# Kernel tuning notes

Hardware: AMD Instinct MI355X
Metric: run time of the kernel (lower is better)

Reference implementation:

```python
import jax, jax.numpy as jnp
import numpy as np
from jax.scipy.fft import dct as jdct, idct as jidct

B, C, L = 512, 64, 512
KEEP_L, KEEP_C = 256, 32          # int(L*0.5), int(C*0.5)
KEEP_L2, KEEP_C2 = 128, 16        # int(KEEP_L*0.5), int(KEEP_C*0.5)


def dct2(x2d):
    # scipy: dct(dct(x, axis=0, norm='ortho'), axis=1, norm='ortho') on (B*C, L)
    return jdct(jdct(x2d, norm='ortho', axis=0), norm='ortho', axis=1)


def idct2(x2d):
    # scipy: idct(idct(X, axis=1, norm='ortho'), axis=0, norm='ortho')
    return jidct(jidct(x2d, norm='ortho', axis=1), norm='ortho', axis=0)


def setup_inputs() -> dict:
    key = jax.random.key(0)
    ks = jax.random.split(key, 7)
    x = jax.random.normal(ks[0], (B, C, L), dtype=jnp.float32)
    W1 = jax.random.normal(ks[1], (L, L), dtype=jnp.float32) / np.sqrt(L)
    b1 = jax.random.normal(ks[2], (L,), dtype=jnp.float32) * 0.01
    W2 = jax.random.normal(ks[3], (KEEP_L, KEEP_L), dtype=jnp.float32) / np.sqrt(KEEP_L)
    b2 = jax.random.normal(ks[4], (KEEP_L,), dtype=jnp.float32) * 0.01
    W3 = jax.random.normal(ks[5], (KEEP_L2, KEEP_L2), dtype=jnp.float32) / np.sqrt(KEEP_L2)
    b3 = jax.random.normal(ks[6], (KEEP_L2,), dtype=jnp.float32) * 0.01
    return {"x": x, "W1": W1, "b1": b1, "W2": W2, "b2": b2, "W3": W3, "b3": b3}


def reference(x, W1, b1, W2, b2, W3, b3):
    Bx, Cx, Lx = x.shape
    # 2D DCT over the flattened (B*C, L) view
    T = dct2(x.reshape(-1, Lx)).reshape(Bx, Cx, Lx)

    # branch 1: Linear over full L
    y1 = T @ W1.T + b1

    # branch 2: Linear over truncated coeffs, zero-pad back to (B, C, L)
    t1 = T[:, :KEEP_C, :KEEP_L]
    y2 = jnp.pad(t1 @ W2.T + b2, ((0, 0), (0, Cx - KEEP_C), (0, Lx - KEEP_L)))

    # branch 3: further truncation
    t2 = T[:, :KEEP_C2, :KEEP_L2]
    y3 = jnp.pad(t2 @ W3.T + b3, ((0, 0), (0, Cx - KEEP_C2), (0, Lx - KEEP_L2)))

    out = jnp.concatenate(
        [idct2(y.reshape(-1, Lx)).reshape(Bx, Cx, Lx) for y in (y1, y2, y3)],
        axis=-1,
    )  # (B, C, 3L)
    return out
```

## Files before the change

### kernel.cpp

```cpp
#include <hip/hip_runtime.h>
#include <cstddef>


#define PI_D 3.14159265358979323846

typedef _Float16 h8 __attribute__((ext_vector_type(8)));
typedef _Float16 h4 __attribute__((ext_vector_type(4)));
typedef float f4 __attribute__((ext_vector_type(4)));

#define MFMA16(a, b, c) __builtin_amdgcn_mfma_f32_16x16x32_f16(a, b, c, 0, 0, 0)

__global__ __launch_bounds__(256) void megafill_k(
    float* __restrict__ F, _Float16* __restrict__ Cmh, _Float16* __restrict__ Smnh,
    _Float16* __restrict__ CmTh, _Float16* __restrict__ SmTh,
    float* __restrict__ v1, float* __restrict__ w2, float* __restrict__ w3,
    const float* __restrict__ b1, const float* __restrict__ b2,
    const float* __restrict__ b3, float* __restrict__ c1, float* __restrict__ c2,
    float* __restrict__ c3) {
  const int blk = blockIdx.x;
  const int tid = threadIdx.x;
  if (blk < 1024) {
    int idx = blk * 256 + tid;
    int k = idx >> 9, m = idx & 511;
    int a = (k * (2 * m + 1)) & 2047;
    float ang = (float)(a * (PI_D / 1024.0));
    float s = (k == 0) ? 0.04419417382415922f : 0.0625f;
    F[idx] = s * cosf(ang);
  } else if (blk < 2048) {
    int idx = (blk - 1024) * 256 + tid;
    int t = idx >> 9, v = idx & 511;
    int a = (t * (2 * v + 1)) & 2047;
    float ang = (float)(a * (PI_D / 1024.0));
    float c = cosf(ang), s = sinf(ang);
    Cmh[idx] = (_Float16)c;
    Smnh[idx] = (_Float16)(-s);
    CmTh[v * 512 + t] = (_Float16)c;
    SmTh[v * 512 + t] = (_Float16)s;
  } else if (blk < 2176) {
    int n = (blk - 2048) * 256 + tid;
    const double s1 = 0.005524271728019903;
    const double s2 = 0.0078125;
    double th = (2 * n + 1) * (PI_D / 65536.0);
    double c = cos(th), s = sin(th);
    double Dr = 1.0 - c, Di = -s;
    double dd = Dr * Dr + Di * Di;
    double Nr = 1.0, Ni = (n & 1) ? 1.0 : -1.0;
    double vre = (Nr * Dr + Ni * Di) / dd;
    v1[n] = (float)(s2 * vre + (s1 - s2));
    int m64 = (2 * n + 1) & 2047;
    double a64 = m64 * (PI_D / 1024.0);
    double D64r = 1.0 - cos(a64), D64i = -sin(a64);
    double d64 = D64r * D64r + D64i * D64i;
    double Gr = (Nr * D64r + Ni * D64i) / d64;
    double Gi = (Ni * D64r - Nr * D64i) / d64;
    int m32 = (2 * n + 1) & 4095;
    double a32 = m32 * (PI_D / 2048.0);
    double S32nr = 1.0 - cos(a32), S32ni = -sin(a32);
    double S32r = (S32nr * Dr + S32ni * Di) / dd;
    double S32i = (S32ni * Dr - S32nr * Di) / dd;
    w2[n] = (float)(s2 * (S32r * Gr - S32i * Gi) + (s1 - s2));
    int m16 = (2 * n + 1) & 8191;
    double a16 = m16 * (PI_D / 4096.0);
    double S16nr = 1.0 - cos(a16), S16ni = -sin(a16);
    double S16r = (S16nr * Dr + S16ni * Di) / dd;
    double S16i = (S16ni * Dr - S16nr * Di) / dd;
    w3[n] = (float)(s2 * (S16r * Gr - S16i * Gi) + (s1 - s2));
  } else {
    int gid = (blk - 2176) * 4 + (tid >> 6);
    int lane = tid & 63;
    int branch = gid >> 9;
    int l = gid & 511;
    int K = 512 >> branch;
    const float* b = (branch == 0) ? b1 : (branch == 1) ? b2 : b3;
    float acc = 0.f;
    for (int m = lane; m < K; m += 64) {
      int a = (m * (2 * l + 1)) & 2047;
      float s = (m == 0) ? 0.04419417382415922f : 0.0625f;
      acc += s * cosf((float)(a * (PI_D / 1024.0))) * b[m];
    }
#pragma unroll
    for (int o = 32; o > 0; o >>= 1) acc += __shfl_down(acc, o, 64);
    if (lane == 0) {
      float* c = (branch == 0) ? c1 : (branch == 1) ? c2 : c3;
      c[l] = acc;
    }
  }
}

__global__ void conv_xh_k(const float* __restrict__ X, _Float16* __restrict__ Xh) {
  int i = blockIdx.x * 256 + threadIdx.x;
  float4 v = ((const float4*)X)[i];
  h4 o;
  o[0] = (_Float16)v.x; o[1] = (_Float16)v.y; o[2] = (_Float16)v.z; o[3] = (_Float16)v.w;
  ((h4*)Xh)[i] = o;
}

__device__ void sgemm_dev(_Float16* As, _Float16* Bs, int bx, int by,
                          const float* __restrict__ A, int lda, int transA,
                          const float* __restrict__ B, int ldb,
                          float* __restrict__ Cf, _Float16* __restrict__ C16,
                          int K, float scale) {
  const int tid = threadIdx.x;
  const int lane = tid & 63;
  const int wm = (tid >> 6) & 1, wn = tid >> 7;
  const int m0 = by * 128, n0 = bx * 128;
  const int fm = lane & 15, fko = (lane >> 4) * 8;
  f4 acc[4][4] = {};
  for (int k0 = 0; k0 < K; k0 += 32) {
    if (transA) {
#pragma unroll
      for (int i = 0; i < 4; i++) {
        int idx4 = tid + i * 256;
        int kk = idx4 & 31, mc = (idx4 >> 5) * 4;
        float4 v = *(const float4*)&A[(size_t)(k0 + kk) * lda + m0 + mc];
        As[(mc + 0) * 40 + kk] = (_Float16)v.x;
        As[(mc + 1) * 40 + kk] = (_Float16)v.y;
        As[(mc + 2) * 40 + kk] = (_Float16)v.z;
        As[(mc + 3) * 40 + kk] = (_Float16)v.w;
      }
    } else {
#pragma unroll
      for (int i = 0; i < 4; i++) {
        int idx4 = tid + i * 256;
        int mm = idx4 >> 3, kc = (idx4 & 7) * 4;
        float4 v = *(const float4*)&A[(size_t)(m0 + mm) * lda + k0 + kc];
        h4 o;
        o[0] = (_Float16)v.x; o[1] = (_Float16)v.y; o[2] = (_Float16)v.z; o[3] = (_Float16)v.w;
        *(h4*)&As[mm * 40 + kc] = o;
      }
    }
#pragma unroll
    for (int i = 0; i < 4; i++) {
      int idx4 = tid + i * 256;
      int kk = idx4 & 31, nc = (idx4 >> 5) * 4;
      float4 v = *(const float4*)&B[(size_t)(k0 + kk) * ldb + n0 + nc];
      Bs[(nc + 0) * 40 + kk] = (_Float16)v.x;
      Bs[(nc + 1) * 40 + kk] = (_Float16)v.y;
      Bs[(nc + 2) * 40 + kk] = (_Float16)v.z;
      Bs[(nc + 3) * 40 + kk] = (_Float16)v.w;
    }
    __syncthreads();
    h8 af[4], bf[4];
#pragma unroll
    for (int i = 0; i < 4; i++) af[i] = *(const h8*)&As[(wm * 64 + i * 16 + fm) * 40 + fko];
#pragma unroll
    for (int j = 0; j < 4; j++) bf[j] = *(const h8*)&Bs[(wn * 64 + j * 16 + fm) * 40 + fko];
#pragma unroll
    for (int i = 0; i < 4; i++)
#pragma unroll
      for (int j = 0; j < 4; j++) acc[i][j] = MFMA16(af[i], bf[j], acc[i][j]);
    __syncthreads();
  }
  const int er = (lane >> 4) * 4, ec = lane & 15;
#pragma unroll
  for (int i = 0; i < 4; i++) {
    int gr0 = m0 + wm * 64 + i * 16 + er;
#pragma unroll
    for (int j = 0; j < 4; j++) {
      int gc = n0 + wn * 64 + j * 16 + ec;
#pragma unroll
      for (int r = 0; r < 4; r++) {
        size_t off = (size_t)(gr0 + r) * 512 + gc;
        if (C16) C16[off] = (_Float16)(acc[i][j][r] * scale);
        else Cf[off] = acc[i][j][r];
      }
    }
  }
}

__global__ __launch_bounds__(256) void sgemm_stage1_k(
    const float* __restrict__ W1, const float* __restrict__ W2,
    const float* __restrict__ W3, const float* __restrict__ F,
    float* __restrict__ Pst, float* __restrict__ Q2, float* __restrict__ Q3) {
  __shared__ _Float16 As[128 * 40];
  __shared__ _Float16 Bs[128 * 40];
  int id = blockIdx.x;
  if (id < 16) {
    sgemm_dev(As, Bs, id & 3, id >> 2, W1, 512, 1, F, 512, Pst, nullptr, 512, 1.f);
  } else if (id < 24) {
    int j = id - 16;
    sgemm_dev(As, Bs, j & 3, j >> 2, W2, 256, 0, F, 512, Q2, nullptr, 256, 1.f);
  } else {
    int j = id - 24;
    sgemm_dev(As, Bs, j & 3, j >> 2, W3, 128, 0, F, 512, Q3, nullptr, 128, 1.f);
  }
}

__global__ __launch_bounds__(256) void sgemm_stage2_k(
    const float* __restrict__ F, const float* __restrict__ Pst,
    const float* __restrict__ Q2, const float* __restrict__ Q3,
    _Float16* __restrict__ M1T, _Float16* __restrict__ M2T,
    _Float16* __restrict__ M3T) {
  __shared__ _Float16 As[128 * 40];
  __shared__ _Float16 Bs[128 * 40];
  int id = blockIdx.x;
  if (id < 16) {
    sgemm_dev(As, Bs, id & 3, id >> 2, Pst, 512, 1, F, 512, nullptr, M1T, 512, 1.f);
  } else if (id < 32) {
    int j = id - 16;
    sgemm_dev(As, Bs, j & 3, j >> 2, F, 512, 1, Q2, 512, nullptr, M2T, 256, 0.0078125f);
  } else {
    int j = id - 32;
    sgemm_dev(As, Bs, j & 3, j >> 2, F, 512, 1, Q3, 512, nullptr, M3T, 128, 0.0078125f);
  }
}

__global__ __launch_bounds__(256) void transpose2_h_k(
    const _Float16* __restrict__ in0, _Float16* __restrict__ out0, int C0,
    const _Float16* __restrict__ in1, _Float16* __restrict__ out1, int C1,
    int xsplit, int R) {
  __shared__ _Float16 t[64][66];
  const _Float16* in;
  _Float16* out;
  int C, bx;
  if ((int)blockIdx.x < xsplit) { in = in0; out = out0; C = C0; bx = blockIdx.x; }
  else { in = in1; out = out1; C = C1; bx = blockIdx.x - xsplit; }
  int tid = threadIdx.x;
  int bxo = bx * 64;
  int by = blockIdx.y * 64;
  int cx = (tid & 15) * 4;
  int ry = tid >> 4;
#pragma unroll
  for (int p = 0; p < 4; p++) {
    int r = ry + p * 16;
    h4 v = *(const h4*)&in[(size_t)(by + r) * C + bxo + cx];
    t[r][cx + 0] = v[0]; t[r][cx + 1] = v[1]; t[r][cx + 2] = v[2]; t[r][cx + 3] = v[3];
  }
  __syncthreads();
#pragma unroll
  for (int p = 0; p < 4; p++) {
    int r2 = ry + p * 16;
    h4 v;
    v[0] = t[cx + 0][r2]; v[1] = t[cx + 1][r2]; v[2] = t[cx + 2][r2]; v[3] = t[cx + 3][r2];
    *(h4*)&out[(size_t)(bxo + r2) * R + by + cx] = v;
  }
}

__device__ __forceinline__ void async16(const _Float16* g, _Float16* l) {
  __builtin_amdgcn_global_load_lds((const __attribute__((address_space(1))) void*)g,
                                   (__attribute__((address_space(3))) void*)l, 16, 0, 0);
}

template <int MODE>
__device__ void gemm_dev(_Float16* As, _Float16* Bs, int bx, int by,
                         const _Float16* __restrict__ A1, const _Float16* __restrict__ A2,
                         const _Float16* __restrict__ B1, const _Float16* __restrict__ B2,
                         void* __restrict__ C1, void* __restrict__ C2, int ldc, int coff,
                         const float* __restrict__ u, const float* __restrict__ wvec,
                         int sb, int tb) {
  constexpr bool DA = (MODE == 1 || MODE == 2);
  constexpr bool DB = (MODE == 1);
  const int tid = threadIdx.x;
  const int lane = tid & 63;
  const int wm = (tid >> 6) & 1, wn = tid >> 7;
  const int m0 = by * 128, n0 = bx * 128;
  const int srow = tid >> 2, scol = (tid & 3) * 8;
  const int mask = (1 << sb) - 1;
  f4 acc[4][4] = {};
  f4 acc2[4][4] = {};
  const int fm = lane & 15, fko = (lane >> 4) * 8;
  for (int k0 = 0; k0 < 512; k0 += 32) {
#pragma unroll
    for (int i = 0; i < 2; i++) {
      int r = m0 + i * 64 + srow;
      int pr = ((r >> sb) << tb) | (r & mask);
      async16(A1 + (size_t)pr * 512 + k0 + scol, &As[i * 2048 + tid * 8]);
      if constexpr (DA)
        async16(A2 + (size_t)pr * 512 + k0 + scol, &As[4096 + i * 2048 + tid * 8]);
      int rb = n0 + i * 64 + srow;
      async16(B1 + (size_t)rb * 512 + k0 + scol, &Bs[i * 2048 + tid * 8]);
      if constexpr (DB)
        async16(B2 + (size_t)rb * 512 + k0 + scol, &Bs[4096 + i * 2048 + tid * 8]);
    }
    __syncthreads();
    h8 af[4], bf[4], af2[4], bf2[4];
#pragma unroll
    for (int i = 0; i < 4; i++) {
      int ro = (wm * 64 + i * 16 + fm) * 32 + fko;
      af[i] = *(const h8*)&As[ro];
      if constexpr (DA) af2[i] = *(const h8*)&As[4096 + ro];
    }
#pragma unroll
    for (int j = 0; j < 4; j++) {
      int co = (wn * 64 + j * 16 + fm) * 32 + fko;
      bf[j] = *(const h8*)&Bs[co];
      if constexpr (DB) bf2[j] = *(const h8*)&Bs[4096 + co];
    }
#pragma unroll
    for (int i = 0; i < 4; i++)
#pragma unroll
      for (int j = 0; j < 4; j++) {
        acc[i][j] = MFMA16(af[i], bf[j], acc[i][j]);
        if constexpr (MODE == 1) acc[i][j] = MFMA16(af2[i], bf2[j], acc[i][j]);
        if constexpr (MODE == 2) acc2[i][j] = MFMA16(af2[i], bf[j], acc2[i][j]);
      }
    __syncthreads();
  }
  const int er = (lane >> 4) * 4, ec = lane & 15;
#pragma unroll
  for (int i = 0; i < 4; i++) {
    int gr0 = m0 + wm * 64 + i * 16 + er;
#pragma unroll
    for (int j = 0; j < 4; j++) {
      int gc = n0 + wn * 64 + j * 16 + ec;
#pragma unroll
      for (int r = 0; r < 4; r++) {
        size_t off = (size_t)(gr0 + r) * ldc + coff + gc;
        if constexpr (MODE == 3) {
          ((float*)C1)[off] = acc[i][j][r] + u[gr0 + r] * wvec[gc];
        } else if constexpr (MODE == 2) {
          ((_Float16*)C1)[off] = (_Float16)acc[i][j][r];
          ((_Float16*)C2)[off] = (_Float16)acc2[i][j][r];
        } else if constexpr (MODE == 1) {
          float v = acc[i][j][r];
          if ((gr0 + r) == 0 && gc < 512) v *= 0.5f;
          ((_Float16*)C1)[off] = (_Float16)v;
        } else {
          ((_Float16*)C1)[off] = (_Float16)acc[i][j][r];
        }
      }
    }
  }
}

template <int MODE>
__global__ __launch_bounds__(256) void mfma_gemm_k(
    const _Float16* __restrict__ A1, const _Float16* __restrict__ A2,
    const _Float16* __restrict__ B1, const _Float16* __restrict__ B2,
    void* __restrict__ C1, void* __restrict__ C2, int ldc, int coff,
    const float* __restrict__ u, const float* __restrict__ wvec, int sb, int tb) {
  __shared__ __align__(16) _Float16 As[((MODE == 1 || MODE == 2) ? 2 : 1) * 4096];
  __shared__ __align__(16) _Float16 Bs[(MODE == 1 ? 2 : 1) * 4096];
  gemm_dev<MODE>(As, Bs, blockIdx.x, blockIdx.y, A1, A2, B1, B2, C1, C2, ldc, coff,
                 u, wvec, sb, tb);
}

__global__ __launch_bounds__(256) void gemm0_pair_k(
    const _Float16* __restrict__ Zh, const _Float16* __restrict__ M2T,
    const _Float16* __restrict__ M3T, _Float16* __restrict__ Y2,
    _Float16* __restrict__ Y3) {
  __shared__ __align__(16) _Float16 As[4096];
  __shared__ __align__(16) _Float16 Bs[4096];
  if ((int)blockIdx.y < 128)
    gemm_dev<0>(As, Bs, blockIdx.x, blockIdx.y, Zh, nullptr, M2T, nullptr, Y2, nullptr,
                512, 0, nullptr, nullptr, 30, 30);
  else
    gemm_dev<0>(As, Bs, blockIdx.x, blockIdx.y - 128, Zh, nullptr, M3T, nullptr, Y3,
                nullptr, 512, 0, nullptr, nullptr, 4, 5);
}

__global__ __launch_bounds__(256) void gemm2_pair_k(
    const _Float16* __restrict__ CmTh, const _Float16* __restrict__ SmTh,
    const _Float16* __restrict__ Y2T, const _Float16* __restrict__ Y3T,
    _Float16* __restrict__ Pc2, _Float16* __restrict__ Ps2,
    _Float16* __restrict__ Pc3, _Float16* __restrict__ Ps3) {
  __shared__ __align__(16) _Float16 As[2 * 4096];
  __shared__ __align__(16) _Float16 Bs[4096];
  if ((int)blockIdx.x < 128)
    gemm_dev<2>(As, Bs, blockIdx.x, blockIdx.y, CmTh, SmTh, Y2T, nullptr, Pc2, Ps2,
                16384, 0, nullptr, nullptr, 30, 30);
  else
    gemm_dev<2>(As, Bs, blockIdx.x - 128, blockIdx.y, CmTh, SmTh, Y3T, nullptr, Pc3,
                Ps3, 8192, 0, nullptr, nullptr, 30, 30);
}

__global__ __launch_bounds__(256) void modmfma_k(
    const _Float16* __restrict__ Xh, _Float16* __restrict__ zc,
    _Float16* __restrict__ zs) {
  __shared__ _Float16 Bs[256 * 72];
  __shared__ _Float16 Ac[32 * 72];
  __shared__ _Float16 As[32 * 72];
  const int tid = threadIdx.x;
  const int lane = tid & 63;
  const int wid = tid >> 6;
  const int vp = blockIdx.y;
  const int l0 = blockIdx.x * 256;
  const float sc = 0.0078125f;
  {
    int r = lane;
    int u = r & 31;
    int n = (r < 32) ? ((u << 10) + vp) : ((u << 10) + 1023 - vp);
    const _Float16* src = Xh + (size_t)n * 512 + l0 + wid * 64;
#pragma unroll
    for (int i = 0; i < 8; i++) {
      h8 v = *(const h8*)(src + i * 8);
      int lb = wid * 64 + i * 8;
#pragma unroll
      for (int e = 0; e < 8; e++) Bs[(lb + e) * 72 + r] = v[e];
    }
  }
  for (int idx = tid; idx < 2048; idx += 256) {
    int kk = idx & 63, j = idx >> 6;
    int u = kk & 31;
    int n = (kk < 32) ? ((u << 10) + vp) : ((u << 10) + 1023 - vp);
    int a = (j * (2 * n + 1)) & 131071;
    float sv, cv;
    __sincosf((float)(a * (PI_D / 65536.0)), &sv, &cv);
    Ac[j * 72 + kk] = (_Float16)(cv * sc);
    As[j * 72 + kk] = (_Float16)(((kk < 32) ? sv : -sv) * sc);
  }
  __syncthreads();
  const int fm = lane & 15, fko = (lane >> 4) * 8;
  f4 accc[2][4] = {};
  f4 accs[2][4] = {};
#pragma unroll
  for (int ks = 0; ks < 2; ks++) {
    int ko = ks * 32 + fko;
    h8 afc[2], afs[2], bf[4];
#pragma unroll
    for (int i = 0; i < 2; i++) {
      afc[i] = *(const h8*)&Ac[(i * 16 + fm) * 72 + ko];
      afs[i] = *(const h8*)&As[(i * 16 + fm) * 72 + ko];
    }
#pragma unroll
    for (int j = 0; j < 4; j++)
      bf[j] = *(const h8*)&Bs[(wid * 64 + j * 16 + fm) * 72 + ko];
#pragma unroll
    for (int i = 0; i < 2; i++)
#pragma unroll
      for (int j = 0; j < 4; j++) {
        accc[i][j] = MFMA16(afc[i], bf[j], accc[i][j]);
        accs[i][j] = MFMA16(afs[i], bf[j], accs[i][j]);
      }
  }
  const int er = (lane >> 4) * 4, ec = lane & 15;
#pragma unroll
  for (int i = 0; i < 2; i++)
#pragma unroll
    for (int j = 0; j < 4; j++)
#pragma unroll
      for (int r = 0; r < 4; r++) {
        int row = i * 16 + er + r;
        int col = l0 + wid * 64 + j * 16 + ec;
        size_t off = (size_t)vp * 16384 + row * 512 + col;
        zc[off] = (_Float16)accc[i][j][r];
        zs[off] = (_Float16)accs[i][j][r];
      }
}

template <int JC>
__device__ void demod_dev(char* smemraw, const _Float16* __restrict__ Pc,
                          const _Float16* __restrict__ Ps,
                          const float* __restrict__ wv, const float* __restrict__ cw,
                          float* __restrict__ out, int coff) {
  constexpr int K2 = 2 * JC;
  constexpr int ST = K2 + 8;
  _Float16* Bs = (_Float16*)smemraw;
  _Float16* At = (_Float16*)(smemraw + (size_t)256 * ST * 2);
  const int tid = threadIdx.x;
  const int lane = tid & 63;
  const int wid = tid >> 6;
  const int vp = blockIdx.y;
  const int l0 = blockIdx.x * 256;
  {
    constexpr int CPL = 64 / K2;
    int r = lane & (K2 - 1);
    int chunk = wid * CPL + (CPL == 1 ? 0 : (lane >> 5));
    int lb = chunk * K2;
    const _Float16* src = (r < JC ? Pc + (size_t)vp * (JC * 512) + r * 512
                                  : Ps + (size_t)vp * (JC * 512) + (r - JC) * 512) +
                          l0 + lb;
#pragma unroll
    for (int i = 0; i < K2 / 8; i++) {
      h8 v = *(const h8*)(src + i * 8);
#pragma unroll
      for (int e = 0; e < 8; e++) Bs[(lb + i * 8 + e) * ST + r] = v[e];
    }
  }
  for (int idx = tid; idx < 64 * K2; idx += 256) {
    int kk = idx & (K2 - 1), m = idx / K2;
    int ab = m >> 5, u = m & 31;
    int n = ab ? ((u << 10) + 1023 - vp) : ((u << 10) + vp);
    int twon = 2 * n + 1;
    float val;
    if (kk < JC) {
      int a = (kk * twon) & 131071;
      val = cosf((float)(a * (PI_D / 65536.0)));
    } else {
      int a = ((kk - JC) * twon) & 131071;
      float sv = sinf((float)(a * (PI_D / 65536.0)));
      val = ab ? sv : -sv;
    }
    At[m * ST + kk] = (_Float16)val;
  }
  __syncthreads();
  const int fm = lane & 15, fko = (lane >> 4) * 8;
  f4 acc[4][4] = {};
#pragma unroll
  for (int ks = 0; ks < K2 / 32; ks++) {
    int ko = ks * 32 + fko;
    h8 af[4], bf[4];
#pragma unroll
    for (int i = 0; i < 4; i++) af[i] = *(const h8*)&At[(i * 16 + fm) * ST + ko];
#pragma unroll
    for (int j = 0; j < 4; j++) bf[j] = *(const h8*)&Bs[(wid * 64 + j * 16 + fm) * ST + ko];
#pragma unroll
    for (int i = 0; i < 4; i++)
#pragma unroll
      for (int j = 0; j < 4; j++) acc[i][j] = MFMA16(af[i], bf[j], acc[i][j]);
  }
  const int er = (lane >> 4) * 4, ec = lane & 15;
#pragma unroll
  for (int i = 0; i < 4; i++)
#pragma unroll
    for (int j = 0; j < 4; j++) {
      int col = l0 + wid * 64 + j * 16 + ec;
      float cl = cw[col];
#pragma unroll
      for (int r = 0; r < 4; r++) {
        int m = i * 16 + er + r;
        int ab = m >> 5, u = m & 31;
        int n = ab ? ((u << 10) + 1023 - vp) : ((u << 10) + vp);
        out[(size_t)n * 1536 + coff + col] = acc[i][j][r] + wv[n] * cl;
      }
    }
}

__global__ __launch_bounds__(256) void demod_pair_k(
    const _Float16* __restrict__ Pc2, const _Float16* __restrict__ Ps2,
    const float* __restrict__ w2v, const float* __restrict__ c2,
    const _Float16* __restrict__ Pc3, const _Float16* __restrict__ Ps3,
    const float* __restrict__ w3v, const float* __restrict__ c3,
    float* __restrict__ out) {
  __shared__ __align__(16) char smem[256 * 72 * 2 + 64 * 72 * 2];
  if (blockIdx.z == 0)
    demod_dev<32>(smem, Pc2, Ps2, w2v, c2, out, 512);
  else
    demod_dev<16>(smem, Pc3, Ps3, w3v, c3, out, 1024);
}

extern "C" void kernel_launch(void* const* d_in, const int* in_sizes, int n_in,
                              void* d_out, int out_size, void* d_ws, size_t ws_size,
                              hipStream_t stream) {
  const float* X  = (const float*)d_in[0];
  const float* W1 = (const float*)d_in[1];
  const float* b1 = (const float*)d_in[2];
  const float* W2 = (const float*)d_in[3];
  const float* b2 = (const float*)d_in[4];
  const float* W3 = (const float*)d_in[5];
  const float* b3 = (const float*)d_in[6];
  float* out = (float*)d_out;
  char* w = (char*)d_ws;
  const size_t MB = 1024 * 1024;

  float* F    = (float*)(w);
  float* v1   = (float*)(w + 9 * MB);
  float* w2v  = (float*)(w + 9 * MB + 131072);
  float* w3v  = (float*)(w + 9 * MB + 262144);
  float* c1   = (float*)(w + 9 * MB + 393216);
  float* c2   = (float*)(w + 9 * MB + 395264);
  float* c3   = (float*)(w + 9 * MB + 397312);
  float* Pst  = (float*)(w + 10 * MB);
  _Float16* CmTh = (_Float16*)(w + 11 * MB);
  _Float16* SmTh = (_Float16*)(w + 11 * MB + 524288);
  _Float16* Cmh  = (_Float16*)(w + 12 * MB);
  _Float16* Smnh = (_Float16*)(w + 12 * MB + 524288);
  _Float16* M1T  = (_Float16*)(w + 13 * MB);
  _Float16* M2T  = (_Float16*)(w + 13 * MB + 524288);
  _Float16* M3T  = (_Float16*)(w + 14 * MB);
  float* Q2      = (float*)(w + 14 * MB + 524288);
  float* Q3      = (float*)(w + 15 * MB);
  _Float16* Xh   = (_Float16*)(w + 16 * MB);
  _Float16* zc   = (_Float16*)(w + 48 * MB);
  _Float16* zs   = (_Float16*)(w + 64 * MB);
  _Float16* Pc2h = (_Float16*)(w + 48 * MB);
  _Float16* Ps2h = (_Float16*)(w + 64 * MB);
  _Float16* Pc3h = (_Float16*)(w + 104 * MB);
  _Float16* Ps3h = (_Float16*)(w + 112 * MB);
  _Float16* zcT  = (_Float16*)(w + 80 * MB);
  _Float16* zsT  = (_Float16*)(w + 96 * MB);
  _Float16* Y2T  = (_Float16*)(w + 80 * MB);
  _Float16* Y3T  = (_Float16*)(w + 96 * MB);
  _Float16* Zh   = (_Float16*)(w + 112 * MB);
  _Float16* Y2   = (_Float16*)(w + 128 * MB);
  _Float16* Y3   = (_Float16*)(w + 144 * MB);

  megafill_k<<<2560, 256, 0, stream>>>(F, Cmh, Smnh, CmTh, SmTh, v1, w2v, w3v,
                                       b1, b2, b3, c1, c2, c3);
  sgemm_stage1_k<<<28, 256, 0, stream>>>(W1, W2, W3, F, Pst, Q2, Q3);
  sgemm_stage2_k<<<48, 256, 0, stream>>>(F, Pst, Q2, Q3, M1T, M2T, M3T);
  conv_xh_k<<<16384, 256, 0, stream>>>(X, Xh);
  modmfma_k<<<dim3(2, 512), 256, 0, stream>>>(Xh, zc, zs);
  transpose2_h_k<<<dim3(512, 8), 256, 0, stream>>>(zc, zcT, 16384, zs, zsT, 16384,
                                                   256, 512);
  mfma_gemm_k<1><<<dim3(128, 4), 256, 0, stream>>>(Cmh, Smnh, zcT, zsT, Zh, nullptr,
                                                   16384, 0, nullptr, nullptr, 30, 30);
  gemm0_pair_k<<<dim3(4, 192), 256, 0, stream>>>(Zh, M2T, M3T, Y2, Y3);
  transpose2_h_k<<<dim3(384, 8), 256, 0, stream>>>(Y2, Y2T, 16384, Y3, Y3T, 8192,
                                                   256, 512);
  gemm2_pair_k<<<dim3(192, 4), 256, 0, stream>>>(CmTh, SmTh, Y2T, Y3T, Pc2h, Ps2h,
                                                 Pc3h, Ps3h);
  demod_pair_k<<<dim3(2, 512, 2), 256, 0, stream>>>(Pc2h, Ps2h, w2v, c2, Pc3h, Ps3h,
                                                    w3v, c3, out);
  mfma_gemm_k<3><<<dim3(4, 256), 256, 0, stream>>>(Xh, nullptr, M1T, nullptr, out,
                                                   nullptr, 1536, 0, v1, c1, 30, 30);
}
```

Before: 588.5 us.

## Fuse setup kernels, drop transposes via k-major B loads, merge final GEMM

The DCT matrix F is now computed on the fly inside the small setup GEMMs instead of being materialized. The fill and stage-1 GEMMs are merged into one launch, and the X conversion and stage-2 GEMMs into another. The two transpose kernels are removed: the MFMA GEMMs read k-major B directly, scattering it into a swizzled LDS layout to avoid bank conflicts. The branch-1 output GEMM is folded into the trio GEMM launch. This cuts launch count and the transpose memory traffic, at the cost of scalar LDS scatter stores, recomputed cosines, and heavier tail blocks in the merged grids.

Measured after the change: 650.9 us. 10.6% more time.

```diff
diff --git a/kernel.cpp b/kernel.cpp
--- a/kernel.cpp
+++ b/kernel.cpp
@@ -10,24 +10,120 @@
 
 #define MFMA16(a, b, c) __builtin_amdgcn_mfma_f32_16x16x32_f16(a, b, c, 0, 0, 0)
 
-__global__ __launch_bounds__(256) void megafill_k(
-    float* __restrict__ F, _Float16* __restrict__ Cmh, _Float16* __restrict__ Smnh,
+__device__ __forceinline__ float Fval(int k, int m) {
+  int a = (k * (2 * m + 1)) & 2047;
+  float s = (k == 0) ? 0.04419417382415922f : 0.0625f;
+  return s * cosf((float)(a * (PI_D / 1024.0)));
+}
+
+__device__ void sgemm_dev(_Float16* As, _Float16* Bs, int bx, int by,
+                          const float* __restrict__ A, int lda, int amode,
+                          const float* __restrict__ B, int ldb, int bmode,
+                          float* __restrict__ Cf, _Float16* __restrict__ C16,
+                          int K, float scale) {
+  const int tid = threadIdx.x;
+  const int lane = tid & 63;
+  const int wm = (tid >> 6) & 1, wn = tid >> 7;
+  const int m0 = by * 128, n0 = bx * 128;
+  const int fm = lane & 15, fko = (lane >> 4) * 8;
+  f4 acc[4][4] = {};
+  for (int k0 = 0; k0 < K; k0 += 32) {
+    if (amode == 1) {
+#pragma unroll
+      for (int i = 0; i < 4; i++) {
+        int idx4 = tid + i * 256;
+        int kk = idx4 & 31, mc = (idx4 >> 5) * 4;
+        float4 v = *(const float4*)&A[(size_t)(k0 + kk) * lda + m0 + mc];
+        As[(mc + 0) * 40 + kk] = (_Float16)v.x;
+        As[(mc + 1) * 40 + kk] = (_Float16)v.y;
+        As[(mc + 2) * 40 + kk] = (_Float16)v.z;
+        As[(mc + 3) * 40 + kk] = (_Float16)v.w;
+      }
+    } else if (amode == 0) {
+#pragma unroll
+      for (int i = 0; i < 4; i++) {
+        int idx4 = tid + i * 256;
+        int mm = idx4 >> 3, kc = (idx4 & 7) * 4;
+        float4 v = *(const float4*)&A[(size_t)(m0 + mm) * lda + k0 + kc];
+        h4 o;
+        o[0] = (_Float16)v.x; o[1] = (_Float16)v.y; o[2] = (_Float16)v.z; o[3] = (_Float16)v.w;
+        *(h4*)&As[mm * 40 + kc] = o;
+      }
+    } else {
+#pragma unroll
+      for (int i = 0; i < 4; i++) {
+        int idx4 = tid + i * 256;
+        int kk = idx4 & 31, mc = (idx4 >> 5) * 4;
+#pragma unroll
+        for (int e = 0; e < 4; e++)
+          As[(mc + e) * 40 + kk] = (_Float16)Fval(k0 + kk, m0 + mc + e);
+      }
+    }
+    if (bmode == 0) {
+#pragma unroll
+      for (int i = 0; i < 4; i++) {
+        int idx4 = tid + i * 256;
+        int kk = idx4 & 31, nc = (idx4 >> 5) * 4;
+        float4 v = *(const float4*)&B[(size_t)(k0 + kk) * ldb + n0 + nc];
+        Bs[(nc + 0) * 40 + kk] = (_Float16)v.x;
+        Bs[(nc + 1) * 40 + kk] = (_Float16)v.y;
+        Bs[(nc + 2) * 40 + kk] = (_Float16)v.z;
+        Bs[(nc + 3) * 40 + kk] = (_Float16)v.w;
+      }
+    } else {
+#pragma unroll
+      for (int i = 0; i < 4; i++) {
+        int idx4 = tid + i * 256;
+        int kk = idx4 & 31, nc = (idx4 >> 5) * 4;
+#pragma unroll
+        for (int e = 0; e < 4; e++)
+          Bs[(nc + e) * 40 + kk] = (_Float16)Fval(k0 + kk, n0 + nc + e);
+      }
+    }
+    __syncthreads();
+    h8 af[4], bf[4];
+#pragma unroll
+    for (int i = 0; i < 4; i++) af[i] = *(const h8*)&As[(wm * 64 + i * 16 + fm) * 40 + fko];
+#pragma unroll
+    for (int j = 0; j < 4; j++) bf[j] = *(const h8*)&Bs[(wn * 64 + j * 16 + fm) * 40 + fko];
+#pragma unroll
+    for (int i = 0; i < 4; i++)
+#pragma unroll
+      for (int j = 0; j < 4; j++) acc[i][j] = MFMA16(af[i], bf[j], acc[i][j]);
+    __syncthreads();
+  }
+  const int er = (lane >> 4) * 4, ec = lane & 15;
+#pragma unroll
+  for (int i = 0; i < 4; i++) {
+    int gr0 = m0 + wm * 64 + i * 16 + er;
+#pragma unroll
+    for (int j = 0; j < 4; j++) {
+      int gc = n0 + wn * 64 + j * 16 + ec;
+#pragma unroll
+      for (int r = 0; r < 4; r++) {
+        size_t off = (size_t)(gr0 + r) * 512 + gc;
+        if (C16) C16[off] = (_Float16)(acc[i][j][r] * scale);
+        else Cf[off] = acc[i][j][r];
+      }
+    }
+  }
+}
+
+__global__ __launch_bounds__(256) void mega1_k(
+    _Float16* __restrict__ Cmh, _Float16* __restrict__ Smnh,
     _Float16* __restrict__ CmTh, _Float16* __restrict__ SmTh,
     float* __restrict__ v1, float* __restrict__ w2, float* __restrict__ w3,
     const float* __restrict__ b1, const float* __restrict__ b2,
     const float* __restrict__ b3, float* __restrict__ c1, float* __restrict__ c2,
-    float* __restrict__ c3) {
+    float* __restrict__ c3, const float* __restrict__ W1,
+    const float* __restrict__ W2, const float* __restrict__ W3,
+    float* __restrict__ Pst, float* __restrict__ Q2, float* __restrict__ Q3) {
+  __shared__ _Float16 As[128 * 40];
+  __shared__ _Float16 Bs[128 * 40];
   const int blk = blockIdx.x;
   const int tid = threadIdx.x;
   if (blk < 1024) {
     int idx = blk * 256 + tid;
-    int k = idx >> 9, m = idx & 511;
-    int a = (k * (2 * m + 1)) & 2047;
-    float ang = (float)(a * (PI_D / 1024.0));
-    float s = (k == 0) ? 0.04419417382415922f : 0.0625f;
-    F[idx] = s * cosf(ang);
-  } else if (blk < 2048) {
-    int idx = (blk - 1024) * 256 + tid;
     int t = idx >> 9, v = idx & 511;
     int a = (t * (2 * v + 1)) & 2047;
     float ang = (float)(a * (PI_D / 1024.0));
@@ -36,8 +132,8 @@
     Smnh[idx] = (_Float16)(-s);
     CmTh[v * 512 + t] = (_Float16)c;
     SmTh[v * 512 + t] = (_Float16)s;
-  } else if (blk < 2176) {
-    int n = (blk - 2048) * 256 + tid;
+  } else if (blk < 1152) {
+    int n = (blk - 1024) * 256 + tid;
     const double s1 = 0.005524271728019903;
     const double s2 = 0.0078125;
     double th = (2 * n + 1) * (PI_D / 65536.0);
@@ -65,174 +161,60 @@
     double S16r = (S16nr * Dr + S16ni * Di) / dd;
     double S16i = (S16ni * Dr - S16nr * Di) / dd;
     w3[n] = (float)(s2 * (S16r * Gr - S16i * Gi) + (s1 - s2));
-  } else {
-    int gid = (blk - 2176) * 4 + (tid >> 6);
+  } else if (blk < 1536) {
+    int gid = (blk - 1152) * 4 + (tid >> 6);
     int lane = tid & 63;
     int branch = gid >> 9;
     int l = gid & 511;
     int K = 512 >> branch;
     const float* b = (branch == 0) ? b1 : (branch == 1) ? b2 : b3;
     float acc = 0.f;
-    for (int m = lane; m < K; m += 64) {
-      int a = (m * (2 * l + 1)) & 2047;
-      float s = (m == 0) ? 0.04419417382415922f : 0.0625f;
-      acc += s * cosf((float)(a * (PI_D / 1024.0))) * b[m];
-    }
+    for (int m = lane; m < K; m += 64) acc += Fval(m, l) * b[m];
 #pragma unroll
     for (int o = 32; o > 0; o >>= 1) acc += __shfl_down(acc, o, 64);
     if (lane == 0) {
       float* c = (branch == 0) ? c1 : (branch == 1) ? c2 : c3;
       c[l] = acc;
     }
-  }
-}
-
-__global__ void conv_xh_k(const float* __restrict__ X, _Float16* __restrict__ Xh) {
-  int i = blockIdx.x * 256 + threadIdx.x;
-  float4 v = ((const float4*)X)[i];
-  h4 o;
-  o[0] = (_Float16)v.x; o[1] = (_Float16)v.y; o[2] = (_Float16)v.z; o[3] = (_Float16)v.w;
-  ((h4*)Xh)[i] = o;
-}
-
-__device__ void sgemm_dev(_Float16* As, _Float16* Bs, int bx, int by,
-                          const float* __restrict__ A, int lda, int transA,
-                          const float* __restrict__ B, int ldb,
-                          float* __restrict__ Cf, _Float16* __restrict__ C16,
-                          int K, float scale) {
-  const int tid = threadIdx.x;
-  const int lane = tid & 63;
-  const int wm = (tid >> 6) & 1, wn = tid >> 7;
-  const int m0 = by * 128, n0 = bx * 128;
-  const int fm = lane & 15, fko = (lane >> 4) * 8;
-  f4 acc[4][4] = {};
-  for (int k0 = 0; k0 < K; k0 += 32) {
-    if (transA) {
-#pragma unroll
-      for (int i = 0; i < 4; i++) {
-        int idx4 = tid + i * 256;
-        int kk = idx4 & 31, mc = (idx4 >> 5) * 4;
-        float4 v = *(const float4*)&A[(size_t)(k0 + kk) * lda + m0 + mc];
-        As[(mc + 0) * 40 + kk] = (_Float16)v.x;
-        As[(mc + 1) * 40 + kk] = (_Float16)v.y;
-        As[(mc + 2) * 40 + kk] = (_Float16)v.z;
-        As[(mc + 3) * 40 + kk] = (_Float16)v.w;
-      }
+  } else {
+    int id = blk - 1536;
+    if (id < 16) {
+      sgemm_dev(As, Bs, id & 3, id >> 2, W1, 512, 1, nullptr, 0, 1, Pst, nullptr, 512, 1.f);
+    } else if (id < 24) {
+      int j = id - 16;
+      sgemm_dev(As, Bs, j & 3, j >> 2, W2, 256, 0, nullptr, 0, 1, Q2, nullptr, 256, 1.f);
     } else {
-#pragma unroll
-      for (int i = 0; i < 4; i++) {
-        int idx4 = tid + i * 256;
-        int mm = idx4 >> 3, kc = (idx4 & 7) * 4;
-        float4 v = *(const float4*)&A[(size_t)(m0 + mm) * lda + k0 + kc];
-        h4 o;
-        o[0] = (_Float16)v.x; o[1] = (_Float16)v.y; o[2] = (_Float16)v.z; o[3] = (_Float16)v.w;
-        *(h4*)&As[mm * 40 + kc] = o;
-      }
-    }
-#pragma unroll
-    for (int i = 0; i < 4; i++) {
-      int idx4 = tid + i * 256;
-      int kk = idx4 & 31, nc = (idx4 >> 5) * 4;
-      float4 v = *(const float4*)&B[(size_t)(k0 + kk) * ldb + n0 + nc];
-      Bs[(nc + 0) * 40 + kk] = (_Float16)v.x;
-      Bs[(nc + 1) * 40 + kk] = (_Float16)v.y;
-      Bs[(nc + 2) * 40 + kk] = (_Float16)v.z;
-      Bs[(nc + 3) * 40 + kk] = (_Float16)v.w;
-    }
-    __syncthreads();
-    h8 af[4], bf[4];
-#pragma unroll
-    for (int i = 0; i < 4; i++) af[i] = *(const h8*)&As[(wm * 64 + i * 16 + fm) * 40 + fko];
-#pragma unroll
-    for (int j = 0; j < 4; j++) bf[j] = *(const h8*)&Bs[(wn * 64 + j * 16 + fm) * 40 + fko];
-#pragma unroll
-    for (int i = 0; i < 4; i++)
-#pragma unroll
-      for (int j = 0; j < 4; j++) acc[i][j] = MFMA16(af[i], bf[j], acc[i][j]);
-    __syncthreads();
-  }
-  const int er = (lane >> 4) * 4, ec = lane & 15;
-#pragma unroll
-  for (int i = 0; i < 4; i++) {
-    int gr0 = m0 + wm * 64 + i * 16 + er;
-#pragma unroll
-    for (int j = 0; j < 4; j++) {
-      int gc = n0 + wn * 64 + j * 16 + ec;
-#pragma unroll
-      for (int r = 0; r < 4; r++) {
-        size_t off = (size_t)(gr0 + r) * 512 + gc;
-        if (C16) C16[off] = (_Float16)(acc[i][j][r] * scale);
-        else Cf[off] = acc[i][j][r];
-      }
-    }
-  }
-}
-
-__global__ __launch_bounds__(256) void sgemm_stage1_k(
-    const float* __restrict__ W1, const float* __restrict__ W2,
-    const float* __restrict__ W3, const float* __restrict__ F,
-    float* __restrict__ Pst, float* __restrict__ Q2, float* __restrict__ Q3) {
+      int j = id - 24;
+      sgemm_dev(As, Bs, j & 3, j >> 2, W3, 128, 0, nullptr, 0, 1, Q3, nullptr, 128, 1.f);
+    }
+  }
+}
+
+__global__ __launch_bounds__(256) void mega2_k(
+    const float* __restrict__ X, _Float16* __restrict__ Xh,
+    const float* __restrict__ Pst, const float* __restrict__ Q2,
+    const float* __restrict__ Q3, _Float16* __restrict__ M1T,
+    _Float16* __restrict__ M2T, _Float16* __restrict__ M3T) {
   __shared__ _Float16 As[128 * 40];
   __shared__ _Float16 Bs[128 * 40];
-  int id = blockIdx.x;
-  if (id < 16) {
-    sgemm_dev(As, Bs, id & 3, id >> 2, W1, 512, 1, F, 512, Pst, nullptr, 512, 1.f);
-  } else if (id < 24) {
-    int j = id - 16;
-    sgemm_dev(As, Bs, j & 3, j >> 2, W2, 256, 0, F, 512, Q2, nullptr, 256, 1.f);
+  const int blk = blockIdx.x;
+  if (blk < 16384) {
+    int i = blk * 256 + threadIdx.x;
+    float4 v = ((const float4*)X)[i];
+    h4 o;
+    o[0] = (_Float16)v.x; o[1] = (_Float16)v.y; o[2] = (_Float16)v.z; o[3] = (_Float16)v.w;
+    ((h4*)Xh)[i] = o;
   } else {
-    int j = id - 24;
-    sgemm_dev(As, Bs, j & 3, j >> 2, W3, 128, 0, F, 512, Q3, nullptr, 128, 1.f);
-  }
-}
-
-__global__ __launch_bounds__(256) void sgemm_stage2_k(
-    const float* __restrict__ F, const float* __restrict__ Pst,
-    const float* __restrict__ Q2, const float* __restrict__ Q3,
-    _Float16* __restrict__ M1T, _Float16* __restrict__ M2T,
-    _Float16* __restrict__ M3T) {
-  __shared__ _Float16 As[128 * 40];
-  __shared__ _Float16 Bs[128 * 40];
-  int id = blockIdx.x;
-  if (id < 16) {
-    sgemm_dev(As, Bs, id & 3, id >> 2, Pst, 512, 1, F, 512, nullptr, M1T, 512, 1.f);
-  } else if (id < 32) {
-    int j = id - 16;
-    sgemm_dev(As, Bs, j & 3, j >> 2, F, 512, 1, Q2, 512, nullptr, M2T, 256, 0.0078125f);
-  } else {
-    int j = id - 32;
-    sgemm_dev(As, Bs, j & 3, j >> 2, F, 512, 1, Q3, 512, nullptr, M3T, 128, 0.0078125f);
-  }
-}
-
-__global__ __launch_bounds__(256) void transpose2_h_k(
-    const _Float16* __restrict__ in0, _Float16* __restrict__ out0, int C0,
-    const _Float16* __restrict__ in1, _Float16* __restrict__ out1, int C1,
-    int xsplit, int R) {
-  __shared__ _Float16 t[64][66];
-  const _Float16* in;
-  _Float16* out;
-  int C, bx;
-  if ((int)blockIdx.x < xsplit) { in = in0; out = out0; C = C0; bx = blockIdx.x; }
-  else { in = in1; out = out1; C = C1; bx = blockIdx.x - xsplit; }
-  int tid = threadIdx.x;
-  int bxo = bx * 64;
-  int by = blockIdx.y * 64;
-  int cx = (tid & 15) * 4;
-  int ry = tid >> 4;
-#pragma unroll
-  for (int p = 0; p < 4; p++) {
-    int r = ry + p * 16;
-    h4 v = *(const h4*)&in[(size_t)(by + r) * C + bxo + cx];
-    t[r][cx + 0] = v[0]; t[r][cx + 1] = v[1]; t[r][cx + 2] = v[2]; t[r][cx + 3] = v[3];
-  }
-  __syncthreads();
-#pragma unroll
-  for (int p = 0; p < 4; p++) {
-    int r2 = ry + p * 16;
-    h4 v;
-    v[0] = t[cx + 0][r2]; v[1] = t[cx + 1][r2]; v[2] = t[cx + 2][r2]; v[3] = t[cx + 3][r2];
-    *(h4*)&out[(size_t)(bxo + r2) * R + by + cx] = v;
+    int id = blk - 16384;
+    if (id < 16) {
+      sgemm_dev(As, Bs, id & 3, id >> 2, Pst, 512, 1, nullptr, 0, 1, nullptr, M1T, 512, 1.f);
+    } else if (id < 32) {
+      int j = id - 16;
+      sgemm_dev(As, Bs, j & 3, j >> 2, nullptr, 0, 2, Q2, 512, 0, nullptr, M2T, 256, 0.0078125f);
+    } else {
+      int j = id - 32;
+      sgemm_dev(As, Bs, j & 3, j >> 2, nullptr, 0, 2, Q3, 512, 0, nullptr, M3T, 128, 0.0078125f);
+    }
   }
 }
 
@@ -241,13 +223,13 @@
                                    (__attribute__((address_space(3))) void*)l, 16, 0, 0);
 }
 
-template <int MODE>
+template <int MODE, bool KMAJ>
 __device__ void gemm_dev(_Float16* As, _Float16* Bs, int bx, int by,
                          const _Float16* __restrict__ A1, const _Float16* __restrict__ A2,
                          const _Float16* __restrict__ B1, const _Float16* __restrict__ B2,
                          void* __restrict__ C1, void* __restrict__ C2, int ldc, int coff,
                          const float* __restrict__ u, const float* __restrict__ wvec,
-                         int sb, int tb) {
+                         int sb, int tb, int ldbK) {
   constexpr bool DA = (MODE == 1 || MODE == 2);
   constexpr bool DB = (MODE == 1);
   const int tid = threadIdx.x;
@@ -267,10 +249,31 @@
       async16(A1 + (size_t)pr * 512 + k0 + scol, &As[i * 2048 + tid * 8]);
       if constexpr (DA)
         async16(A2 + (size_t)pr * 512 + k0 + scol, &As[4096 + i * 2048 + tid * 8]);
-      int rb = n0 + i * 64 + srow;
-      async16(B1 + (size_t)rb * 512 + k0 + scol, &Bs[i * 2048 + tid * 8]);
-      if constexpr (DB)
-        async16(B2 + (size_t)rb * 512 + k0 + scol, &Bs[4096 + i * 2048 + tid * 8]);
+      if constexpr (!KMAJ) {
+        int rb = n0 + i * 64 + srow;
+        async16(B1 + (size_t)rb * 512 + k0 + scol, &Bs[i * 2048 + tid * 8]);
+        if constexpr (DB)
+          async16(B2 + (size_t)rb * 512 + k0 + scol, &Bs[4096 + i * 2048 + tid * 8]);
+      }
+    }
+    if constexpr (KMAJ) {
+#pragma unroll
+      for (int t = 0; t < 2; t++) {
+        int idx = tid + t * 256;
+        int kk = idx >> 4;
+        int nl0 = (idx & 15) * 8;
+        h8 v = *(const h8*)&B1[(size_t)(k0 + kk) * ldbK + n0 + nl0];
+        h8 v2;
+        if constexpr (DB) v2 = *(const h8*)&B2[(size_t)(k0 + kk) * ldbK + n0 + nl0];
+        int klo = kk & 7, khi = kk >> 3;
+#pragma unroll
+        for (int e = 0; e < 8; e++) {
+          int nl = nl0 + e;
+          int ch = khi ^ ((nl >> 3) & 3);
+          Bs[nl * 32 + ch * 8 + klo] = v[e];
+          if constexpr (DB) Bs[4096 + nl * 32 + ch * 8 + klo] = v2[e];
+        }
+      }
     }
     __syncthreads();
     h8 af[4], bf[4], af2[4], bf2[4];
@@ -282,7 +285,14 @@
     }
 #pragma unroll
     for (int j = 0; j < 4; j++) {
-      int co = (wn * 64 + j * 16 + fm) * 32 + fko;
+      int rr = wn * 64 + j * 16 + fm;
+      int co;
+      if constexpr (KMAJ) {
+        int ch = (lane >> 4) ^ ((rr >> 3) & 3);
+        co = rr * 32 + ch * 8;
+      } else {
+        co = rr * 32 + fko;
+      }
       bf[j] = *(const h8*)&Bs[co];
       if constexpr (DB) bf2[j] = *(const h8*)&Bs[4096 + co];
     }
@@ -323,45 +333,52 @@
   }
 }
 
-template <int MODE>
+template <int MODE, bool KMAJ>
 __global__ __launch_bounds__(256) void mfma_gemm_k(
     const _Float16* __restrict__ A1, const _Float16* __restrict__ A2,
     const _Float16* __restrict__ B1, const _Float16* __restrict__ B2,
     void* __restrict__ C1, void* __restrict__ C2, int ldc, int coff,
-    const float* __restrict__ u, const float* __restrict__ wvec, int sb, int tb) {
+    const float* __restrict__ u, const float* __restrict__ wvec, int sb, int tb,
+    int ldbK) {
   __shared__ __align__(16) _Float16 As[((MODE == 1 || MODE == 2) ? 2 : 1) * 4096];
   __shared__ __align__(16) _Float16 Bs[(MODE == 1 ? 2 : 1) * 4096];
-  gemm_dev<MODE>(As, Bs, blockIdx.x, blockIdx.y, A1, A2, B1, B2, C1, C2, ldc, coff,
-                 u, wvec, sb, tb);
-}
-
-__global__ __launch_bounds__(256) void gemm0_pair_k(
+  gemm_dev<MODE, KMAJ>(As, Bs, blockIdx.x, blockIdx.y, A1, A2, B1, B2, C1, C2, ldc,
+                       coff, u, wvec, sb, tb, ldbK);
+}
+
+__global__ __launch_bounds__(256) void gemm_trio_k(
     const _Float16* __restrict__ Zh, const _Float16* __restrict__ M2T,
     const _Float16* __restrict__ M3T, _Float16* __restrict__ Y2,
-    _Float16* __restrict__ Y3) {
+    _Float16* __restrict__ Y3, const _Float16* __restrict__ Xh,
+    const _Float16* __restrict__ M1T, float* __restrict__ out,
+    const float* __restrict__ v1, const float* __restrict__ c1) {
   __shared__ __align__(16) _Float16 As[4096];
   __shared__ __align__(16) _Float16 Bs[4096];
-  if ((int)blockIdx.y < 128)
-    gemm_dev<0>(As, Bs, blockIdx.x, blockIdx.y, Zh, nullptr, M2T, nullptr, Y2, nullptr,
-                512, 0, nullptr, nullptr, 30, 30);
+  int by = blockIdx.y;
+  if (by < 128)
+    gemm_dev<0, false>(As, Bs, blockIdx.x, by, Zh, nullptr, M2T, nullptr, Y2, nullptr,
+                       512, 0, nullptr, nullptr, 30, 30, 0);
+  else if (by < 192)
+    gemm_dev<0, false>(As, Bs, blockIdx.x, by - 128, Zh, nullptr, M3T, nullptr, Y3,
+                       nullptr, 512, 0, nullptr, nullptr, 4, 5, 0);
   else
-    gemm_dev<0>(As, Bs, blockIdx.x, blockIdx.y - 128, Zh, nullptr, M3T, nullptr, Y3,
-                nullptr, 512, 0, nullptr, nullptr, 4, 5);
+    gemm_dev<3, false>(As, Bs, blockIdx.x, by - 192, Xh, nullptr, M1T, nullptr, out,
+                       nullptr, 1536, 0, v1, c1, 30, 30, 0);
 }
 
 __global__ __launch_bounds__(256) void gemm2_pair_k(
     const _Float16* __restrict__ CmTh, const _Float16* __restrict__ SmTh,
-    const _Float16* __restrict__ Y2T, const _Float16* __restrict__ Y3T,
+    const _Float16* __restrict__ Y2, const _Float16* __restrict__ Y3,
     _Float16* __restrict__ Pc2, _Float16* __restrict__ Ps2,
     _Float16* __restrict__ Pc3, _Float16* __restrict__ Ps3) {
   __shared__ __align__(16) _Float16 As[2 * 4096];
   __shared__ __align__(16) _Float16 Bs[4096];
   if ((int)blockIdx.x < 128)
-    gemm_dev<2>(As, Bs, blockIdx.x, blockIdx.y, CmTh, SmTh, Y2T, nullptr, Pc2, Ps2,
-                16384, 0, nullptr, nullptr, 30, 30);
+    gemm_dev<2, true>(As, Bs, blockIdx.x, blockIdx.y, CmTh, SmTh, Y2, nullptr, Pc2,
+                      Ps2, 16384, 0, nullptr, nullptr, 30, 30, 16384);
   else
-    gemm_dev<2>(As, Bs, blockIdx.x - 128, blockIdx.y, CmTh, SmTh, Y3T, nullptr, Pc3,
-                Ps3, 8192, 0, nullptr, nullptr, 30, 30);
+    gemm_dev<2, true>(As, Bs, blockIdx.x - 128, blockIdx.y, CmTh, SmTh, Y3, nullptr,
+                      Pc3, Ps3, 8192, 0, nullptr, nullptr, 30, 30, 8192);
 }
 
 __global__ __launch_bounds__(256) void modmfma_k(
@@ -543,7 +560,6 @@
   char* w = (char*)d_ws;
   const size_t MB = 1024 * 1024;
 
-  float* F    = (float*)(w);
   float* v1   = (float*)(w + 9 * MB);
   float* w2v  = (float*)(w + 9 * MB + 131072);
   float* w3v  = (float*)(w + 9 * MB + 262144);
@@ -567,31 +583,20 @@
   _Float16* Ps2h = (_Float16*)(w + 64 * MB);
   _Float16* Pc3h = (_Float16*)(w + 104 * MB);
   _Float16* Ps3h = (_Float16*)(w + 112 * MB);
-  _Float16* zcT  = (_Float16*)(w + 80 * MB);
-  _Float16* zsT  = (_Float16*)(w + 96 * MB);
-  _Float16* Y2T  = (_Float16*)(w + 80 * MB);
-  _Float16* Y3T  = (_Float16*)(w + 96 * MB);
   _Float16* Zh   = (_Float16*)(w + 112 * MB);
   _Float16* Y2   = (_Float16*)(w + 128 * MB);
   _Float16* Y3   = (_Float16*)(w + 144 * MB);
 
-  megafill_k<<<2560, 256, 0, stream>>>(F, Cmh, Smnh, CmTh, SmTh, v1, w2v, w3v,
-                                       b1, b2, b3, c1, c2, c3);
-  sgemm_stage1_k<<<28, 256, 0, stream>>>(W1, W2, W3, F, Pst, Q2, Q3);
-  sgemm_stage2_k<<<48, 256, 0, stream>>>(F, Pst, Q2, Q3, M1T, M2T, M3T);
-  conv_xh_k<<<16384, 256, 0, stream>>>(X, Xh);
+  mega1_k<<<1564, 256, 0, stream>>>(Cmh, Smnh, CmTh, SmTh, v1, w2v, w3v,
+                                    b1, b2, b3, c1, c2, c3, W1, W2, W3, Pst, Q2, Q3);
+  mega2_k<<<16432, 256, 0, stream>>>(X, Xh, Pst, Q2, Q3, M1T, M2T, M3T);
   modmfma_k<<<dim3(2, 512), 256, 0, stream>>>(Xh, zc, zs);
-  transpose2_h_k<<<dim3(512, 8), 256, 0, stream>>>(zc, zcT, 16384, zs, zsT, 16384,
-                                                   256, 512);
-  mfma_gemm_k<1><<<dim3(128, 4), 256, 0, stream>>>(Cmh, Smnh, zcT, zsT, Zh, nullptr,
-                                                   16384, 0, nullptr, nullptr, 30, 30);
-  gemm0_pair_k<<<dim3(4, 192), 256, 0, stream>>>(Zh, M2T, M3T, Y2, Y3);
-  transpose2_h_k<<<dim3(384, 8), 256, 0, stream>>>(Y2, Y2T, 16384, Y3, Y3T, 8192,
-                                                   256, 512);
-  gemm2_pair_k<<<dim3(192, 4), 256, 0, stream>>>(CmTh, SmTh, Y2T, Y3T, Pc2h, Ps2h,
+  mfma_gemm_k<1, true><<<dim3(128, 4), 256, 0, stream>>>(
+      Cmh, Smnh, zc, zs, Zh, nullptr, 16384, 0, nullptr, nullptr, 30, 30, 16384);
+  gemm_trio_k<<<dim3(4, 448), 256, 0, stream>>>(Zh, M2T, M3T, Y2, Y3, Xh, M1T, out,
+                                                v1, c1);
+  gemm2_pair_k<<<dim3(192, 4), 256, 0, stream>>>(CmTh, SmTh, Y2, Y3, Pc2h, Ps2h,
                                                  Pc3h, Ps3h);
   demod_pair_k<<<dim3(2, 512, 2), 256, 0, stream>>>(Pc2h, Ps2h, w2v, c2, Pc3h, Ps3h,
                                                     w3v, c3, out);
-  mfma_gemm_k<3><<<dim3(4, 256), 256, 0, stream>>>(Xh, nullptr, M1T, nullptr, out,
-                                                   nullptr, 1536, 0, v1, c1, 30, 30);
-}
+}
```
